# Kernel tuning notes

Hardware: AMD Instinct MI355X
Metric: run time of the kernel (lower is better)

## Reference

```python
import jax, jax.numpy as jnp
import numpy as np

KS = 3   # kernel_size = sqrt(window_size=9)
PAD = 1  # KS // 2


def _unfold(t):
    # F.unfold(t, kernel_size=3, padding=1) then view(B,C,K,HW).permute(0,3,2,1)
    # -> (B, HW, K, C), K enumerated row-major over the 3x3 window.
    B, C, H, W = t.shape
    tp = jnp.pad(t, ((0, 0), (0, 0), (PAD, PAD), (PAD, PAD)))
    patches = jnp.stack(
        [tp[:, :, i:i + H, j:j + W] for i in range(KS) for j in range(KS)],
        axis=2,
    )  # (B, C, K, H, W)
    return patches.reshape(B, C, KS * KS, H * W).transpose(0, 3, 2, 1)


def setup_inputs() -> dict:
    key = jax.random.key(0)
    ks = jax.random.split(key, 8)
    B, C, H, W = 8, 256, 64, 64
    Cr = C // 8  # reduction=8
    return {
        "x": jax.random.normal(ks[0], (B, C, H, W), dtype=jnp.float32),
        "Wq": jax.random.normal(ks[1], (Cr, C), dtype=jnp.float32) * 0.02,
        "bq": jax.random.normal(ks[2], (Cr,), dtype=jnp.float32) * 0.02,
        "Wk": jax.random.normal(ks[3], (Cr, C), dtype=jnp.float32) * 0.02,
        "bk": jax.random.normal(ks[4], (Cr,), dtype=jnp.float32) * 0.02,
        "Wv": jax.random.normal(ks[5], (C, C), dtype=jnp.float32) * 0.02,
        "bv": jax.random.normal(ks[6], (C,), dtype=jnp.float32) * 0.02,
        "gamma": jax.random.normal(ks[7], (1,), dtype=jnp.float32) * 0.1,
    }


def reference(x, Wq, bq, Wk, bk, Wv, bv, gamma):
    B, C, H, W = x.shape
    # 1x1 convs == per-pixel linear projections
    q = jnp.einsum('bchw,oc->bohw', x, Wq) + bq[None, :, None, None]
    k = jnp.einsum('bchw,oc->bohw', x, Wk) + bk[None, :, None, None]
    v = jnp.einsum('bchw,oc->bohw', x, Wv) + bv[None, :, None, None]
    ku = _unfold(k)  # (B, HW, K, Cr)
    vu = _unfold(v)  # (B, HW, K, C)
    qf = q.reshape(B, -1, H * W).transpose(0, 2, 1)  # (B, HW, Cr)
    energy = jnp.einsum('bqc,bqkc->bqk', qf, ku)     # (B, HW, K)
    attn = jax.nn.softmax(energy, axis=-1)
    out = jnp.einsum('bqk,bqkc->bqc', attn, vu)      # (B, HW, C)
    out = out.transpose(0, 2, 1).reshape(B, C, H, W)
    return gamma * out + x
```

## Files before the change

### kernel.cpp

```cpp
#include <hip/hip_runtime.h>

#define HW   4096
#define HIMG 64
#define WIMG 64
#define CC   256
#define CR   32
#define B_   8

typedef __attribute__((ext_vector_type(8))) short bf16x8;
typedef __attribute__((ext_vector_type(4))) float f32x4;

__device__ inline unsigned short f2bf(float f) {
    union { float f; unsigned u; } v; v.f = f;
    return (unsigned short)((v.u + 0x8000u) >> 16);
}
__device__ inline float bf2f(unsigned short h) {
    union { unsigned u; float f; } v; v.u = ((unsigned)h) << 16; return v.f;
}
__device__ inline unsigned pack2(float a, float b) {
    return (unsigned)f2bf(a) | ((unsigned)f2bf(b) << 16);
}

__global__ __launch_bounds__(256) void wconv(
    const float* __restrict__ Wq, const float* __restrict__ bq,
    const float* __restrict__ Wk, const float* __restrict__ bk,
    const float* __restrict__ Wv, const float* __restrict__ bv,
    unsigned short* __restrict__ Wb, float* __restrict__ bb)
{
    const int o = blockIdx.x;
    const float* src; const float* bsrc; int orel;
    if (o < 32)      { src = Wq; bsrc = bq; orel = o;      }
    else if (o < 64) { src = Wk; bsrc = bk; orel = o - 32; }
    else             { src = Wv; bsrc = bv; orel = o - 64; }
    Wb[o * CC + threadIdx.x] = f2bf(src[orel * CC + threadIdx.x]);
    if (threadIdx.x == 0) bb[o] = bsrc[orel];
}

__global__ __launch_bounds__(256) void proj_gemm(
    const unsigned short* __restrict__ Wb, const float* __restrict__ bb,
    const float* __restrict__ x,
    float* __restrict__ q, float* __restrict__ k,
    unsigned short* __restrict__ vv)
{
    __shared__ unsigned short As[320 * 72];
    __shared__ float          xt32[64 * 65];
    __shared__ unsigned short Bs[64 * 64];

    const int b   = blockIdx.y;
    const int hw0 = blockIdx.x * 64;
    const int t    = threadIdx.x;
    const int lane = t & 63, wv = t >> 6;
    const int m16  = lane & 15, quad = lane >> 4;

    f32x4 acc[5][4];
    #pragma unroll
    for (int i = 0; i < 5; ++i)
        #pragma unroll
        for (int n = 0; n < 4; ++n)
            acc[i][n] = (f32x4){0.f, 0.f, 0.f, 0.f};

    for (int kc = 0; kc < 4; ++kc) {
        const int k0 = kc * 64;
        if (kc) __syncthreads();

        #pragma unroll
        for (int i = 0; i < 10; ++i) {
            int idx = t + 256 * i;
            int row = idx >> 3, s8 = idx & 7;
            *(uint4*)&As[row * 72 + s8 * 8] =
                *(const uint4*)&Wb[row * CC + k0 + s8 * 8];
        }
        #pragma unroll
        for (int i = 0; i < 4; ++i) {
            int idx = t + 256 * i;
            int c = idx >> 4, p4 = (idx & 15) * 4;
            float4 vx = *(const float4*)&x[((size_t)b * CC + k0 + c) * HW + hw0 + p4];
            *(float4*)&xt32[c * 65 + p4] = vx;
        }
        __syncthreads();

        {
            const int px = lane;
            const int c0 = wv * 16;
            float f[16];
            #pragma unroll
            for (int j = 0; j < 16; ++j)
                f[j] = xt32[(c0 + j) * 65 + px];
            uint4 w0, w1;
            w0.x = pack2(f[0],  f[1]);  w0.y = pack2(f[2],  f[3]);
            w0.z = pack2(f[4],  f[5]);  w0.w = pack2(f[6],  f[7]);
            w1.x = pack2(f[8],  f[9]);  w1.y = pack2(f[10], f[11]);
            w1.z = pack2(f[12], f[13]); w1.w = pack2(f[14], f[15]);
            const int lg0 = c0 >> 3, sw = px & 7;
            *(uint4*)&Bs[px * 64 + ((lg0     ^ sw) * 8)] = w0;
            *(uint4*)&Bs[px * 64 + (((lg0+1) ^ sw) * 8)] = w1;
        }
        __syncthreads();

        #pragma unroll
        for (int ks = 0; ks < 2; ++ks) {
            bf16x8 af[5], bf[4];
            #pragma unroll
            for (int i = 0; i < 5; ++i)
                af[i] = *(const bf16x8*)&As[((wv * 5 + i) * 16 + m16) * 72
                                            + ks * 32 + quad * 8];
            #pragma unroll
            for (int n = 0; n < 4; ++n) {
                int px = n * 16 + m16;
                int lg = ks * 4 + quad;
                bf[n] = *(const bf16x8*)&Bs[px * 64 + ((lg ^ (px & 7)) * 8)];
            }
            #pragma unroll
            for (int i = 0; i < 5; ++i)
                #pragma unroll
                for (int n = 0; n < 4; ++n)
                    acc[i][n] = __builtin_amdgcn_mfma_f32_16x16x32_bf16(
                        af[i], bf[n], acc[i][n], 0, 0, 0);
        }
    }

    #pragma unroll
    for (int i = 0; i < 5; ++i) {
        const int ob = (wv * 5 + i) * 16;
        #pragma unroll
        for (int r = 0; r < 4; ++r) {
            const int orow = quad * 4 + r;
            const float bias = bb[ob + orow];
            if (ob < 64) {
                float* dst = (ob < 32) ? q : k;
                int orel = (ob < 32) ? ob : ob - 32;
                size_t rowbase = ((size_t)b * CR + orel + orow) * HW;
                #pragma unroll
                for (int n = 0; n < 4; ++n)
                    dst[rowbase + hw0 + n * 16 + m16] = acc[i][n][r] + bias;
            } else {
                size_t rowbase = ((size_t)b * CC + (ob - 64) + orow) * HW;
                #pragma unroll
                for (int n = 0; n < 4; ++n)
                    vv[rowbase + hw0 + n * 16 + m16] = f2bf(acc[i][n][r] + bias);
            }
        }
    }
}

__global__ __launch_bounds__(256) void attn_w(
    const float* __restrict__ q_, const float* __restrict__ k_,
    float* __restrict__ aw)
{
    __shared__ float qs[64][33];
    __shared__ float ks[3][64][33];
    __shared__ float es[64][9];
    const int h = blockIdx.x, b = blockIdx.y, t = threadIdx.x;

    #pragma unroll
    for (int i = 0; i < 2; ++i) {
        int idx = t + 256 * i, cr = idx >> 4, p4 = (idx & 15) * 4;
        float4 vq = *(const float4*)&q_[((size_t)b * CR + cr) * HW + h * WIMG + p4];
        qs[p4 + 0][cr] = vq.x; qs[p4 + 1][cr] = vq.y;
        qs[p4 + 2][cr] = vq.z; qs[p4 + 3][cr] = vq.w;
    }
    #pragma unroll
    for (int r = 0; r < 3; ++r) {
        int hh = h + r - 1;
        bool ok = (hh >= 0) && (hh < HIMG);
        #pragma unroll
        for (int i = 0; i < 2; ++i) {
            int idx = t + 256 * i, cr = idx >> 4, p4 = (idx & 15) * 4;
            float4 vk = make_float4(0.f, 0.f, 0.f, 0.f);
            if (ok)
                vk = *(const float4*)&k_[((size_t)b * CR + cr) * HW + hh * WIMG + p4];
            ks[r][p4 + 0][cr] = vk.x; ks[r][p4 + 1][cr] = vk.y;
            ks[r][p4 + 2][cr] = vk.z; ks[r][p4 + 3][cr] = vk.w;
        }
    }
    __syncthreads();

    for (int id = t; id < 576; id += 256) {
        int px = id / 9, kk = id - px * 9;
        int di = kk / 3, dj = kk - di * 3;
        int hh = h + di - 1, ww = px + dj - 1;
        float e = 0.f;
        if (hh >= 0 && hh < HIMG && ww >= 0 && ww < WIMG) {
            float s = 0.f;
            #pragma unroll
            for (int c = 0; c < CR; ++c) s = fmaf(qs[px][c], ks[di][ww][c], s);
            e = s;
        }
        es[px][kk] = e;
    }
    __syncthreads();

    if (t < 64) {
        float m = es[t][0];
        #pragma unroll
        for (int kk = 1; kk < 9; ++kk) m = fmaxf(m, es[t][kk]);
        float ex[9]; float ssum = 0.f;
        #pragma unroll
        for (int kk = 0; kk < 9; ++kk) { ex[kk] = __expf(es[t][kk] - m); ssum += ex[kk]; }
        float inv = 1.f / ssum;
        float* dst = &aw[((size_t)b * HW + h * WIMG + t) * 12];
        #pragma unroll
        for (int kk = 0; kk < 9; ++kk) dst[kk] = ex[kk] * inv;
    }
}

__global__ __launch_bounds__(256) void apply(
    const float* __restrict__ x, const unsigned short* __restrict__ vv,
    const float* __restrict__ aw, const float* __restrict__ gamma,
    float* __restrict__ out)
{
    __shared__ float vs[3][32][72];
    __shared__ float aws[64][12];
    const int h = blockIdx.x, cb = blockIdx.y, b = blockIdx.z, t = threadIdx.x;

    if (t < 192) {
        int px = t / 3, seg = t - px * 3;
        *(float4*)&aws[px][seg * 4] =
            *(const float4*)&aw[((size_t)b * HW + h * WIMG + px) * 12 + seg * 4];
    }
    #pragma unroll
    for (int i = 0; i < 6; ++i) {
        int idx = t + 256 * i;
        int p4 = (idx & 15) * 4, c = (idx >> 4) & 31, r = idx >> 9;
        int hh = h + r - 1;
        float4 val = make_float4(0.f, 0.f, 0.f, 0.f);
        if (hh >= 0 && hh < HIMG) {
            ushort4 u = *(const ushort4*)&vv[((size_t)b * CC + cb * 32 + c) * HW
                                             + hh * WIMG + p4];
            val = make_float4(bf2f(u.x), bf2f(u.y), bf2f(u.z), bf2f(u.w));
        }
        *(float4*)&vs[r][c][4 + p4] = val;
    }
    if (t < 96) {
        int r = t >> 5, c = t & 31;
        float4 z = make_float4(0.f, 0.f, 0.f, 0.f);
        *(float4*)&vs[r][c][0]  = z;
        *(float4*)&vs[r][c][68] = z;
    }
    __syncthreads();

    const int px0 = (t & 15) * 4;
    const int cl  = t >> 4;
    float w[4][9];
    #pragma unroll
    for (int i = 0; i < 4; ++i)
        #pragma unroll
        for (int kk = 0; kk < 9; ++kk) w[i][kk] = aws[px0 + i][kk];
    const float g = gamma[0];

    #pragma unroll
    for (int ci = 0; ci < 2; ++ci) {
        int c = cl + 16 * ci;
        float a0 = 0.f, a1 = 0.f, a2 = 0.f, a3 = 0.f;
        #pragma unroll
        for (int r = 0; r < 3; ++r) {
            float4 ctr = *(float4*)&vs[r][c][4 + px0];
            float  lft = vs[r][c][3 + px0];
            float  rgt = vs[r][c][8 + px0];
            int r3 = r * 3;
            a0 = fmaf(w[0][r3], lft,   fmaf(w[0][r3+1], ctr.x, fmaf(w[0][r3+2], ctr.y, a0)));
            a1 = fmaf(w[1][r3], ctr.x, fmaf(w[1][r3+1], ctr.y, fmaf(w[1][r3+2], ctr.z, a1)));
            a2 = fmaf(w[2][r3], ctr.y, fmaf(w[2][r3+1], ctr.z, fmaf(w[2][r3+2], ctr.w, a2)));
            a3 = fmaf(w[3][r3], ctr.z, fmaf(w[3][r3+1], ctr.w, fmaf(w[3][r3+2], rgt,  a3)));
        }
        size_t base = ((size_t)b * CC + cb * 32 + c) * HW + h * WIMG + px0;
        float4 xa = *(const float4*)&x[base];
        float4 o;
        o.x = fmaf(g, a0, xa.x); o.y = fmaf(g, a1, xa.y);
        o.z = fmaf(g, a2, xa.z); o.w = fmaf(g, a3, xa.w);
        *(float4*)&out[base] = o;
    }
}

extern "C" void kernel_launch(void* const* d_in, const int* in_sizes, int n_in,
                              void* d_out, int out_size, void* d_ws, size_t ws_size,
                              hipStream_t stream)
{
    const float* x     = (const float*)d_in[0];
    const float* Wq    = (const float*)d_in[1];
    const float* bq    = (const float*)d_in[2];
    const float* Wk    = (const float*)d_in[3];
    const float* bk    = (const float*)d_in[4];
    const float* Wv    = (const float*)d_in[5];
    const float* bv    = (const float*)d_in[6];
    const float* gamma = (const float*)d_in[7];
    float* out = (float*)d_out;

    float* q  = (float*)d_ws;
    float* k  = q + (size_t)B_ * CR * HW;
    unsigned short* vv = (unsigned short*)(k + (size_t)B_ * CR * HW);
    float* aw = (float*)(vv + (size_t)B_ * CC * HW);
    unsigned short* Wb = (unsigned short*)(aw + (size_t)B_ * HW * 12);
    float* bb = (float*)(Wb + 320 * CC);

    wconv<<<dim3(320), 256, 0, stream>>>(Wq, bq, Wk, bk, Wv, bv, Wb, bb);
    proj_gemm<<<dim3(HW / 64, B_), 256, 0, stream>>>(Wb, bb, x, q, k, vv);
    attn_w<<<dim3(HIMG, B_), 256, 0, stream>>>(q, k, aw);
    apply<<<dim3(HIMG, CC / 32, B_), 256, 0, stream>>>(x, vv, aw, gamma, out);
}
```

Measured before the change: 134.7 us.

## Fuse attention-weight and apply kernels into one kernel with shared memory union

Merges attn_w and apply into a single attn_apply kernel, so softmax weights stay in shared memory instead of going through a global aw buffer. Each block now covers one image row for all 256 channels, staging V in bf16 in two 128-channel chunks, with the stage reusing the Q/K buffers through a union. It also permutes the row index, which changes which rows run together. The gain is one fewer launch and no aw round trip, but the grid shrinks from 4096 to 512 blocks of 512 threads, which cuts parallelism and adds serialized staging barriers.

```diff
diff --git a/kernel.cpp b/kernel.cpp
--- a/kernel.cpp
+++ b/kernel.cpp
@@ -143,39 +143,42 @@
     }
 }
 
-__global__ __launch_bounds__(256) void attn_w(
+__global__ __launch_bounds__(512) void attn_apply(
     const float* __restrict__ q_, const float* __restrict__ k_,
-    float* __restrict__ aw)
-{
-    __shared__ float qs[64][33];
-    __shared__ float ks[3][64][33];
+    const unsigned short* __restrict__ vv,
+    const float* __restrict__ x, const float* __restrict__ gamma,
+    float* __restrict__ out)
+{
+    __shared__ union SM {
+        struct { float qs[64][33]; float ks[3][64][33]; } e;
+        unsigned short vs[3][128][72];
+    } sm;
     __shared__ float es[64][9];
-    const int h = blockIdx.x, b = blockIdx.y, t = threadIdx.x;
-
-    #pragma unroll
-    for (int i = 0; i < 2; ++i) {
-        int idx = t + 256 * i, cr = idx >> 4, p4 = (idx & 15) * 4;
+    __shared__ float aws[64][12];
+
+    const int t  = threadIdx.x;
+    const int hx = blockIdx.x;
+    const int h  = ((hx & 7) << 3) | (hx >> 3);
+    const int b  = blockIdx.y;
+
+    {
+        const int cr = t >> 4, p4 = (t & 15) * 4;
         float4 vq = *(const float4*)&q_[((size_t)b * CR + cr) * HW + h * WIMG + p4];
-        qs[p4 + 0][cr] = vq.x; qs[p4 + 1][cr] = vq.y;
-        qs[p4 + 2][cr] = vq.z; qs[p4 + 3][cr] = vq.w;
-    }
-    #pragma unroll
-    for (int r = 0; r < 3; ++r) {
-        int hh = h + r - 1;
-        bool ok = (hh >= 0) && (hh < HIMG);
-        #pragma unroll
-        for (int i = 0; i < 2; ++i) {
-            int idx = t + 256 * i, cr = idx >> 4, p4 = (idx & 15) * 4;
+        sm.e.qs[p4 + 0][cr] = vq.x; sm.e.qs[p4 + 1][cr] = vq.y;
+        sm.e.qs[p4 + 2][cr] = vq.z; sm.e.qs[p4 + 3][cr] = vq.w;
+        #pragma unroll
+        for (int r = 0; r < 3; ++r) {
+            int hh = h + r - 1;
             float4 vk = make_float4(0.f, 0.f, 0.f, 0.f);
-            if (ok)
+            if (hh >= 0 && hh < HIMG)
                 vk = *(const float4*)&k_[((size_t)b * CR + cr) * HW + hh * WIMG + p4];
-            ks[r][p4 + 0][cr] = vk.x; ks[r][p4 + 1][cr] = vk.y;
-            ks[r][p4 + 2][cr] = vk.z; ks[r][p4 + 3][cr] = vk.w;
+            sm.e.ks[r][p4 + 0][cr] = vk.x; sm.e.ks[r][p4 + 1][cr] = vk.y;
+            sm.e.ks[r][p4 + 2][cr] = vk.z; sm.e.ks[r][p4 + 3][cr] = vk.w;
         }
     }
     __syncthreads();
 
-    for (int id = t; id < 576; id += 256) {
+    for (int id = t; id < 576; id += 512) {
         int px = id / 9, kk = id - px * 9;
         int di = kk / 3, dj = kk - di * 3;
         int hh = h + di - 1, ww = px + dj - 1;
@@ -183,7 +186,8 @@
         if (hh >= 0 && hh < HIMG && ww >= 0 && ww < WIMG) {
             float s = 0.f;
             #pragma unroll
-            for (int c = 0; c < CR; ++c) s = fmaf(qs[px][c], ks[di][ww][c], s);
+            for (int c = 0; c < CR; ++c)
+                s = fmaf(sm.e.qs[px][c], sm.e.ks[di][ww][c], s);
             e = s;
         }
         es[px][kk] = e;
@@ -198,77 +202,72 @@
         #pragma unroll
         for (int kk = 0; kk < 9; ++kk) { ex[kk] = __expf(es[t][kk] - m); ssum += ex[kk]; }
         float inv = 1.f / ssum;
-        float* dst = &aw[((size_t)b * HW + h * WIMG + t) * 12];
-        #pragma unroll
-        for (int kk = 0; kk < 9; ++kk) dst[kk] = ex[kk] * inv;
-    }
-}
-
-__global__ __launch_bounds__(256) void apply(
-    const float* __restrict__ x, const unsigned short* __restrict__ vv,
-    const float* __restrict__ aw, const float* __restrict__ gamma,
-    float* __restrict__ out)
-{
-    __shared__ float vs[3][32][72];
-    __shared__ float aws[64][12];
-    const int h = blockIdx.x, cb = blockIdx.y, b = blockIdx.z, t = threadIdx.x;
-
-    if (t < 192) {
-        int px = t / 3, seg = t - px * 3;
-        *(float4*)&aws[px][seg * 4] =
-            *(const float4*)&aw[((size_t)b * HW + h * WIMG + px) * 12 + seg * 4];
-    }
-    #pragma unroll
-    for (int i = 0; i < 6; ++i) {
-        int idx = t + 256 * i;
-        int p4 = (idx & 15) * 4, c = (idx >> 4) & 31, r = idx >> 9;
-        int hh = h + r - 1;
-        float4 val = make_float4(0.f, 0.f, 0.f, 0.f);
-        if (hh >= 0 && hh < HIMG) {
-            ushort4 u = *(const ushort4*)&vv[((size_t)b * CC + cb * 32 + c) * HW
-                                             + hh * WIMG + p4];
-            val = make_float4(bf2f(u.x), bf2f(u.y), bf2f(u.z), bf2f(u.w));
-        }
-        *(float4*)&vs[r][c][4 + p4] = val;
-    }
-    if (t < 96) {
-        int r = t >> 5, c = t & 31;
-        float4 z = make_float4(0.f, 0.f, 0.f, 0.f);
-        *(float4*)&vs[r][c][0]  = z;
-        *(float4*)&vs[r][c][68] = z;
-    }
+        #pragma unroll
+        for (int kk = 0; kk < 9; ++kk) aws[t][kk] = ex[kk] * inv;
+    }
+
+    auto stage_v = [&](int cc) {
+        #pragma unroll
+        for (int i = 0; i < 12; ++i) {
+            int idx = t + 512 * i;
+            int p4 = (idx & 15) * 4;
+            int c  = (idx >> 4) & 127;
+            int r  = idx >> 11;
+            int hh = h + r - 1;
+            ushort4 u = make_ushort4(0, 0, 0, 0);
+            if (hh >= 0 && hh < HIMG)
+                u = *(const ushort4*)&vv[((size_t)b * CC + cc * 128 + c) * HW
+                                          + hh * WIMG + p4];
+            *(ushort4*)&sm.vs[r][c][4 + p4] = u;
+        }
+        if (t < 384) {
+            int r = t >> 7, c = t & 127;
+            ushort4 z = make_ushort4(0, 0, 0, 0);
+            *(ushort4*)&sm.vs[r][c][0]  = z;
+            *(ushort4*)&sm.vs[r][c][68] = z;
+        }
+    };
+
+    stage_v(0);
     __syncthreads();
 
     const int px0 = (t & 15) * 4;
     const int cl  = t >> 4;
+    const float g = gamma[0];
     float w[4][9];
     #pragma unroll
     for (int i = 0; i < 4; ++i)
         #pragma unroll
         for (int kk = 0; kk < 9; ++kk) w[i][kk] = aws[px0 + i][kk];
-    const float g = gamma[0];
-
-    #pragma unroll
-    for (int ci = 0; ci < 2; ++ci) {
-        int c = cl + 16 * ci;
-        float a0 = 0.f, a1 = 0.f, a2 = 0.f, a3 = 0.f;
-        #pragma unroll
-        for (int r = 0; r < 3; ++r) {
-            float4 ctr = *(float4*)&vs[r][c][4 + px0];
-            float  lft = vs[r][c][3 + px0];
-            float  rgt = vs[r][c][8 + px0];
-            int r3 = r * 3;
-            a0 = fmaf(w[0][r3], lft,   fmaf(w[0][r3+1], ctr.x, fmaf(w[0][r3+2], ctr.y, a0)));
-            a1 = fmaf(w[1][r3], ctr.x, fmaf(w[1][r3+1], ctr.y, fmaf(w[1][r3+2], ctr.z, a1)));
-            a2 = fmaf(w[2][r3], ctr.y, fmaf(w[2][r3+1], ctr.z, fmaf(w[2][r3+2], ctr.w, a2)));
-            a3 = fmaf(w[3][r3], ctr.z, fmaf(w[3][r3+1], ctr.w, fmaf(w[3][r3+2], rgt,  a3)));
-        }
-        size_t base = ((size_t)b * CC + cb * 32 + c) * HW + h * WIMG + px0;
-        float4 xa = *(const float4*)&x[base];
-        float4 o;
-        o.x = fmaf(g, a0, xa.x); o.y = fmaf(g, a1, xa.y);
-        o.z = fmaf(g, a2, xa.z); o.w = fmaf(g, a3, xa.w);
-        *(float4*)&out[base] = o;
+
+    #pragma unroll
+    for (int cc = 0; cc < 2; ++cc) {
+        if (cc) { __syncthreads(); stage_v(1); __syncthreads(); }
+        #pragma unroll
+        for (int ci = 0; ci < 4; ++ci) {
+            int c = cl + 32 * ci;
+            float a0 = 0.f, a1 = 0.f, a2 = 0.f, a3 = 0.f;
+            #pragma unroll
+            for (int r = 0; r < 3; ++r) {
+                const unsigned short* row = &sm.vs[r][c][0];
+                ushort4 uc = *(const ushort4*)&row[4 + px0];
+                float c0 = bf2f(uc.x), c1 = bf2f(uc.y);
+                float c2 = bf2f(uc.z), c3 = bf2f(uc.w);
+                float lft = bf2f(row[3 + px0]);
+                float rgt = bf2f(row[8 + px0]);
+                int r3 = r * 3;
+                a0 = fmaf(w[0][r3], lft, fmaf(w[0][r3+1], c0, fmaf(w[0][r3+2], c1, a0)));
+                a1 = fmaf(w[1][r3], c0,  fmaf(w[1][r3+1], c1, fmaf(w[1][r3+2], c2, a1)));
+                a2 = fmaf(w[2][r3], c1,  fmaf(w[2][r3+1], c2, fmaf(w[2][r3+2], c3, a2)));
+                a3 = fmaf(w[3][r3], c2,  fmaf(w[3][r3+1], c3, fmaf(w[3][r3+2], rgt, a3)));
+            }
+            size_t base = ((size_t)b * CC + cc * 128 + c) * HW + h * WIMG + px0;
+            float4 xa = *(const float4*)&x[base];
+            float4 o;
+            o.x = fmaf(g, a0, xa.x); o.y = fmaf(g, a1, xa.y);
+            o.z = fmaf(g, a2, xa.z); o.w = fmaf(g, a3, xa.w);
+            *(float4*)&out[base] = o;
+        }
     }
 }
 
@@ -289,12 +288,10 @@
     float* q  = (float*)d_ws;
     float* k  = q + (size_t)B_ * CR * HW;
     unsigned short* vv = (unsigned short*)(k + (size_t)B_ * CR * HW);
-    float* aw = (float*)(vv + (size_t)B_ * CC * HW);
-    unsigned short* Wb = (unsigned short*)(aw + (size_t)B_ * HW * 12);
+    unsigned short* Wb = vv + (size_t)B_ * CC * HW;
     float* bb = (float*)(Wb + 320 * CC);
 
     wconv<<<dim3(320), 256, 0, stream>>>(Wq, bq, Wk, bk, Wv, bv, Wb, bb);
     proj_gemm<<<dim3(HW / 64, B_), 256, 0, stream>>>(Wb, bb, x, q, k, vv);
-    attn_w<<<dim3(HIMG, B_), 256, 0, stream>>>(q, k, aw);
-    apply<<<dim3(HIMG, CC / 32, B_), 256, 0, stream>>>(x, vv, aw, gamma, out);
-}
+    attn_apply<<<dim3(HIMG, B_), 512, 0, stream>>>(q, k, vv, x, gamma, out);
+}
```

Result: no change. 135.4 us (+0.5%).

## Load projection GEMM operands directly from global memory, dropping LDS staging

Applied to the files above, without the earlier changes.

The projection GEMM no longer stages the weight tile and transposed input tile through shared memory. Each lane now reads its MFMA A-fragment straight from the bf16 weight buffer, and gathers eight strided fp32 x values per B-fragment straight from global memory, converting them to bf16 in registers. This removes LDS traffic and three barriers per K-chunk. In exchange it issues many scalar strided global loads (stride HW), loses coalescing and reuse across waves, and relies on cache hits for the weight reads.

```diff
diff --git a/kernel.cpp b/kernel.cpp
--- a/kernel.cpp
+++ b/kernel.cpp
@@ -42,10 +42,6 @@
     float* __restrict__ q, float* __restrict__ k,
     unsigned short* __restrict__ vv)
 {
-    __shared__ unsigned short As[320 * 72];
-    __shared__ float          xt32[64 * 65];
-    __shared__ unsigned short Bs[64 * 64];
-
     const int b   = blockIdx.y;
     const int hw0 = blockIdx.x * 64;
     const int t    = threadIdx.x;
@@ -59,57 +55,35 @@
         for (int n = 0; n < 4; ++n)
             acc[i][n] = (f32x4){0.f, 0.f, 0.f, 0.f};
 
+    const float* xb = x + (size_t)b * CC * HW + hw0;
+
+    #pragma unroll
     for (int kc = 0; kc < 4; ++kc) {
-        const int k0 = kc * 64;
-        if (kc) __syncthreads();
-
-        #pragma unroll
-        for (int i = 0; i < 10; ++i) {
-            int idx = t + 256 * i;
-            int row = idx >> 3, s8 = idx & 7;
-            *(uint4*)&As[row * 72 + s8 * 8] =
-                *(const uint4*)&Wb[row * CC + k0 + s8 * 8];
-        }
-        #pragma unroll
-        for (int i = 0; i < 4; ++i) {
-            int idx = t + 256 * i;
-            int c = idx >> 4, p4 = (idx & 15) * 4;
-            float4 vx = *(const float4*)&x[((size_t)b * CC + k0 + c) * HW + hw0 + p4];
-            *(float4*)&xt32[c * 65 + p4] = vx;
-        }
-        __syncthreads();
-
-        {
-            const int px = lane;
-            const int c0 = wv * 16;
-            float f[16];
-            #pragma unroll
-            for (int j = 0; j < 16; ++j)
-                f[j] = xt32[(c0 + j) * 65 + px];
-            uint4 w0, w1;
-            w0.x = pack2(f[0],  f[1]);  w0.y = pack2(f[2],  f[3]);
-            w0.z = pack2(f[4],  f[5]);  w0.w = pack2(f[6],  f[7]);
-            w1.x = pack2(f[8],  f[9]);  w1.y = pack2(f[10], f[11]);
-            w1.z = pack2(f[12], f[13]); w1.w = pack2(f[14], f[15]);
-            const int lg0 = c0 >> 3, sw = px & 7;
-            *(uint4*)&Bs[px * 64 + ((lg0     ^ sw) * 8)] = w0;
-            *(uint4*)&Bs[px * 64 + (((lg0+1) ^ sw) * 8)] = w1;
-        }
-        __syncthreads();
-
         #pragma unroll
         for (int ks = 0; ks < 2; ++ks) {
-            bf16x8 af[5], bf[4];
+            const int c0 = kc * 64 + ks * 32 + quad * 8;
+
+            bf16x8 af[5];
             #pragma unroll
             for (int i = 0; i < 5; ++i)
-                af[i] = *(const bf16x8*)&As[((wv * 5 + i) * 16 + m16) * 72
-                                            + ks * 32 + quad * 8];
+                af[i] = *(const bf16x8*)&Wb[((wv * 5 + i) * 16 + m16) * CC + c0];
+
+            bf16x8 bf[4];
             #pragma unroll
             for (int n = 0; n < 4; ++n) {
-                int px = n * 16 + m16;
-                int lg = ks * 4 + quad;
-                bf[n] = *(const bf16x8*)&Bs[px * 64 + ((lg ^ (px & 7)) * 8)];
+                const float* xp = xb + n * 16 + m16;
+                float f[8];
+                #pragma unroll
+                for (int j = 0; j < 8; ++j)
+                    f[j] = xp[(size_t)(c0 + j) * HW];
+                union { bf16x8 v; unsigned u[4]; } tmp;
+                tmp.u[0] = pack2(f[0], f[1]);
+                tmp.u[1] = pack2(f[2], f[3]);
+                tmp.u[2] = pack2(f[4], f[5]);
+                tmp.u[3] = pack2(f[6], f[7]);
+                bf[n] = tmp.v;
             }
+
             #pragma unroll
             for (int i = 0; i < 5; ++i)
                 #pragma unroll
```

After: 143.8 us. 6.8% more time.
